# Kernel tuning notes

Measured on AMD Instinct MI355X. Metric: run time of the kernel, lower is better.

Reference implementation:

```python
import jax, jax.numpy as jnp
import numpy as np

D_MODEL = 1024
NUM_HEADS = 16
HEAD_DIM = D_MODEL // NUM_HEADS
D_FF = 4096
B, S = 4, 2048
EPS = 1e-5


def layernorm(x, gamma, beta):
    mu = jnp.mean(x, axis=-1, keepdims=True)
    var = jnp.mean(jnp.square(x - mu), axis=-1, keepdims=True)
    return (x - mu) * jax.lax.rsqrt(var + EPS) * gamma + beta


def setup_inputs() -> dict:
    key = jax.random.key(0)
    ks = jax.random.split(key, 16)
    s_in = 1.0 / np.sqrt(D_MODEL)
    s_ff = 1.0 / np.sqrt(D_FF)
    return {
        "x": jax.random.normal(ks[0], (B, S, D_MODEL), jnp.float32),
        "Wq": jax.random.normal(ks[1], (D_MODEL, D_MODEL), jnp.float32) * s_in,
        "bq": jnp.zeros((D_MODEL,), jnp.float32),
        "Wk": jax.random.normal(ks[2], (D_MODEL, D_MODEL), jnp.float32) * s_in,
        "bk": jnp.zeros((D_MODEL,), jnp.float32),
        "Wv": jax.random.normal(ks[3], (D_MODEL, D_MODEL), jnp.float32) * s_in,
        "bv": jnp.zeros((D_MODEL,), jnp.float32),
        "Wo": jax.random.normal(ks[4], (D_MODEL, D_MODEL), jnp.float32) * s_in,
        "bo": jnp.zeros((D_MODEL,), jnp.float32),
        "W1": jax.random.normal(ks[5], (D_MODEL, D_FF), jnp.float32) * s_in,
        "b1": jnp.zeros((D_FF,), jnp.float32),
        "W2": jax.random.normal(ks[6], (D_FF, D_MODEL), jnp.float32) * s_ff,
        "b2": jnp.zeros((D_MODEL,), jnp.float32),
        "g1": jnp.ones((D_MODEL,), jnp.float32),
        "be1": jnp.zeros((D_MODEL,), jnp.float32),
        "g2": jnp.ones((D_MODEL,), jnp.float32),
        "be2": jnp.zeros((D_MODEL,), jnp.float32),
    }


def reference(x, Wq, bq, Wk, bk, Wv, bv, Wo, bo, W1, b1, W2, b2, g1, be1, g2, be2):
    # multi-head self-attention (dropout is identity at eval)
    def split_heads(t):  # [B,S,D] -> [B,H,S,hd]
        return t.reshape(B, S, NUM_HEADS, HEAD_DIM).transpose(0, 2, 1, 3)

    q = split_heads(x @ Wq + bq)
    k = split_heads(x @ Wk + bk)
    v = split_heads(x @ Wv + bv)
    scores = jnp.einsum("bhqd,bhkd->bhqk", q, k) / np.sqrt(HEAD_DIM)
    attn = jax.nn.softmax(scores, axis=-1)
    out = jnp.einsum("bhqk,bhkd->bhqd", attn, v)
    out = out.transpose(0, 2, 1, 3).reshape(B, S, D_MODEL)
    attn_out = out @ Wo + bo

    h = layernorm(x + attn_out, g1, be1)
    ff = jax.nn.relu(h @ W1 + b1) @ W2 + b2
    return layernorm(h + ff, g2, be2)
```

## Files before the change

### kernel.cpp

```cpp
#include <hip/hip_runtime.h>
#include <hip/hip_bf16.h>


#define DM    1024
#define DFF   4096
#define NH    16
#define HD    64
#define BATCH 4
#define SEQ   2048
#define TOK   (BATCH * SEQ)

typedef __attribute__((ext_vector_type(8))) __bf16 bf16x8;
typedef __attribute__((ext_vector_type(4))) float f32x4;
typedef __attribute__((ext_vector_type(16))) float f32x16;
typedef __attribute__((ext_vector_type(4))) unsigned short u16x4;

typedef const __attribute__((address_space(1))) unsigned int* gas1_t;
typedef __attribute__((address_space(3))) unsigned int* las3_t;

__device__ __forceinline__ void gl_lds16(const void* g, void* l) {
  __builtin_amdgcn_global_load_lds((gas1_t)g, (las3_t)l, 16, 0, 0);
}

__device__ __forceinline__ unsigned short f2bu(float x) {
  return __builtin_bit_cast(unsigned short, __float2bfloat16(x));
}

__device__ __forceinline__ unsigned pk_bf16_trunc(float hi, float lo) {
  return __builtin_amdgcn_perm(__builtin_bit_cast(unsigned, hi),
                               __builtin_bit_cast(unsigned, lo), 0x07060302u);
}

__global__ __launch_bounds__(256) void cast_bf16(
    const float* __restrict__ in, unsigned short* __restrict__ out, int n4) {
  int i = blockIdx.x * 256 + threadIdx.x;
  if (i >= n4) return;
  float4 v = ((const float4*)in)[i];
  u16x4 o = {f2bu(v.x), f2bu(v.y), f2bu(v.z), f2bu(v.w)};
  ((u16x4*)out)[i] = o;
}

__global__ __launch_bounds__(256) void transpose_cast(
    const float* __restrict__ in, unsigned short* __restrict__ out, int K, int N) {
  __shared__ float tile[32][33];
  int n0 = blockIdx.x * 32, k0 = blockIdx.y * 32;
  int tx = threadIdx.x, ty = threadIdx.y;
#pragma unroll
  for (int i = 0; i < 4; ++i)
    tile[ty + 8 * i][tx] = in[(size_t)(k0 + ty + 8 * i) * N + n0 + tx];
  __syncthreads();
#pragma unroll
  for (int i = 0; i < 4; ++i)
    out[(size_t)(n0 + ty + 8 * i) * K + k0 + tx] = f2bu(tile[tx][ty + 8 * i]);
}

__global__ __launch_bounds__(256) void transpose_cast4(
    const float* __restrict__ A0, const float* __restrict__ A1,
    const float* __restrict__ A2, const float* __restrict__ A3,
    unsigned short* __restrict__ O0, unsigned short* __restrict__ O1,
    unsigned short* __restrict__ O2, unsigned short* __restrict__ O3) {
  __shared__ float tile[32][33];
  const float* in; unsigned short* out;
  switch (blockIdx.z) {
    case 0: in = A0; out = O0; break;
    case 1: in = A1; out = O1; break;
    case 2: in = A2; out = O2; break;
    default: in = A3; out = O3; break;
  }
  int n0 = blockIdx.x * 32, k0 = blockIdx.y * 32;
  int tx = threadIdx.x, ty = threadIdx.y;
#pragma unroll
  for (int i = 0; i < 4; ++i)
    tile[ty + 8 * i][tx] = in[(size_t)(k0 + ty + 8 * i) * DM + n0 + tx];
  __syncthreads();
#pragma unroll
  for (int i = 0; i < 4; ++i)
    out[(size_t)(n0 + ty + 8 * i) * DM + k0 + tx] = f2bu(tile[tx][ty + 8 * i]);
}

template <int QM, int QN>
__device__ __forceinline__ void phase_mma(
    const unsigned short* As, const unsigned short* Bs, int bufofs,
    int wr, int wc, int l31, int khalf, f32x16 acc[2][2][2]) {
  const char* Ah = (const char*)(As + bufofs + QM * 8192);
  const char* Bh = (const char*)(Bs + bufofs + QN * 8192);
  const int rA0 = wr * 64 + l31, rA1 = rA0 + 32, rB = wc * 32 + l31;
  bf16x8 a0[4], a1[4], bb[4];
#pragma unroll
  for (int ks = 0; ks < 4; ++ks) {
    const int c = ks * 2 + khalf;
    a0[ks] = *(const bf16x8*)(Ah + rA0 * 128 + ((c ^ (rA0 & 7)) << 4));
    a1[ks] = *(const bf16x8*)(Ah + rA1 * 128 + ((c ^ (rA1 & 7)) << 4));
    bb[ks] = *(const bf16x8*)(Bh + rB * 128 + ((c ^ (rB & 7)) << 4));
  }
  __builtin_amdgcn_s_setprio(1);
#pragma unroll
  for (int ks = 0; ks < 4; ++ks) {
    acc[QM][QN][0] = __builtin_amdgcn_mfma_f32_32x32x16_bf16(
        a0[ks], bb[ks], acc[QM][QN][0], 0, 0, 0);
    acc[QM][QN][1] = __builtin_amdgcn_mfma_f32_32x32x16_bf16(
        a1[ks], bb[ks], acc[QM][QN][1], 0, 0, 0);
  }
  __builtin_amdgcn_s_setprio(0);
}

__device__ __forceinline__ void mainloop256(
    const unsigned short* __restrict__ A, int lda,
    const unsigned short* __restrict__ Bt, int ldb, int Kl,
    int m0, int n0, unsigned short* As, unsigned short* Bs,
    f32x16 acc[2][2][2]) {
  const int tid = threadIdx.x, lane = tid & 63, w = tid >> 6;
  const int l31 = lane & 31, khalf = lane >> 5;
  const int wr = w >> 2, wc = w & 3;

  const unsigned short* pa[2][2];
  const unsigned short* pb[2][2];
#pragma unroll
  for (int h = 0; h < 2; ++h)
#pragma unroll
    for (int i = 0; i < 2; ++i) {
      const int g = (i * 8 + w) * 64 + lane;
      const int r = g >> 3;
      const int cs = ((g & 7) ^ (r & 7)) * 8;
      pa[h][i] = A + (size_t)(m0 + h * 128 + r) * lda + cs;
      pb[h][i] = Bt + (size_t)(n0 + h * 128 + r) * ldb + cs;
    }
  const int wofs = w * 512;

#define STA(BUF, H, I) gl_lds16(pa[H][I], As + (BUF) * 16384 + (H) * 8192 + (I) * 4096 + wofs)
#define STB(BUF, H, I) gl_lds16(pb[H][I], Bs + (BUF) * 16384 + (H) * 8192 + (I) * 4096 + wofs)
#define ADV_A(H) { pa[H][0] += 64; pa[H][1] += 64; }
#define ADV_B(H) { pb[H][0] += 64; pb[H][1] += 64; }

  STA(0, 0, 0); STA(0, 0, 1); ADV_A(0);
  STB(0, 0, 0); STB(0, 0, 1); ADV_B(0);
  STB(0, 1, 0); STB(0, 1, 1); ADV_B(1);
  STA(0, 1, 0); STA(0, 1, 1); ADV_A(1);

#define PH(BUF, QMv, QNv, WAITSTR, STG)                                  \
  asm volatile(WAITSTR ::: "memory");                                    \
  STG;                                                                   \
  phase_mma<QMv, QNv>(As, Bs, (BUF) * 16384, wr, wc, l31, khalf, acc)

#define TILE_STEADY(B)                                                        \
  PH(B, 0, 0, "s_waitcnt vmcnt(4)\n\ts_barrier",                              \
     { STA(B ^ 1, 0, 0); STA(B ^ 1, 0, 1); ADV_A(0); });                      \
  PH(B, 0, 1, "s_waitcnt vmcnt(4)\n\ts_barrier",                              \
     { STB(B ^ 1, 0, 0); STB(B ^ 1, 0, 1); ADV_B(0); });                      \
  PH(B, 1, 0, "s_waitcnt vmcnt(4)\n\ts_barrier",                              \
     { STB(B ^ 1, 1, 0); STB(B ^ 1, 1, 1); ADV_B(1); });                      \
  PH(B, 1, 1, "s_barrier",                                                    \
     { STA(B ^ 1, 1, 0); STA(B ^ 1, 1, 1); ADV_A(1); })

  const int NT = Kl >> 6;
  for (int t = 0; t + 2 < NT; t += 2) {
    TILE_STEADY(0);
    TILE_STEADY(1);
  }
  TILE_STEADY(0);
  PH(1, 0, 0, "s_waitcnt vmcnt(4)\n\ts_barrier", {});
  PH(1, 0, 1, "s_waitcnt vmcnt(2)\n\ts_barrier", {});
  PH(1, 1, 0, "s_waitcnt vmcnt(0)\n\ts_barrier", {});
  PH(1, 1, 1, "s_barrier", {});

#undef TILE_STEADY
#undef PH
#undef ADV_B
#undef ADV_A
#undef STB
#undef STA
}


__global__ __launch_bounds__(512, 2) void gemm256(
    const unsigned short* __restrict__ A, int lda,
    const unsigned short* __restrict__ Bt, int ldb, int Kl,
    const float* __restrict__ bias, void* __restrict__ C0,
    void* __restrict__ C1, int N, float alpha, int relu, int ofp32) {
  __shared__ unsigned short As[32768];
  __shared__ unsigned short Bs[32768];
  const int tid = threadIdx.x, lane = tid & 63, w = tid >> 6;
  const int l31 = lane & 31, khalf = lane >> 5;
  const int wr = w >> 2, wc = w & 3;
  const int m0 = blockIdx.y * 256, n0 = blockIdx.x * 256;
  const int koff = blockIdx.z * Kl;
  void* Cout = blockIdx.z ? C1 : C0;
  const float* be = blockIdx.z ? nullptr : bias;

  f32x16 acc[2][2][2];
#pragma unroll
  for (int qm = 0; qm < 2; ++qm)
#pragma unroll
    for (int qn = 0; qn < 2; ++qn)
#pragma unroll
      for (int mi = 0; mi < 2; ++mi)
#pragma unroll
        for (int r = 0; r < 16; ++r) acc[qm][qn][mi][r] = 0.f;

  mainloop256(A + koff, lda, Bt + koff, ldb, Kl, m0, n0, As, Bs, acc);

#pragma unroll
  for (int qn = 0; qn < 2; ++qn) {
    const int col = n0 + qn * 128 + wc * 32 + l31;
    const float bvv = be ? be[col] : 0.f;
#pragma unroll
    for (int qm = 0; qm < 2; ++qm)
#pragma unroll
      for (int mi = 0; mi < 2; ++mi) {
#pragma unroll
        for (int g = 0; g < 4; ++g) {
          const int rbase = m0 + qm * 128 + wr * 64 + mi * 32 + g * 8 + khalf * 4;
#pragma unroll
          for (int r = 0; r < 4; ++r) {
            float val = alpha * (acc[qm][qn][mi][g * 4 + r] + bvv);
            if (relu) val = fmaxf(val, 0.f);
            size_t idx = (size_t)(rbase + r) * N + col;
            if (ofp32) ((float*)Cout)[idx] = val;
            else ((unsigned short*)Cout)[idx] = f2bu(val);
          }
        }
      }
  }
}

#define QSCALE 0.18033688f

__global__ __launch_bounds__(512, 2) void gemm_qkv256(
    const unsigned short* __restrict__ A, const unsigned short* __restrict__ Bt,
    const float* __restrict__ bq, const float* __restrict__ bk,
    const float* __restrict__ bv,
    unsigned short* __restrict__ Qb, unsigned short* __restrict__ Kb,
    unsigned short* __restrict__ Vtg) {
  __shared__ unsigned short As[32768];
  __shared__ unsigned short Bs[32768];
  const int tid = threadIdx.x, lane = tid & 63, w = tid >> 6;
  const int l31 = lane & 31, khalf = lane >> 5;
  const int wr = w >> 2, wc = w & 3;
  const int m0 = blockIdx.y * 256, n0 = blockIdx.x * 256;

  f32x16 acc[2][2][2];
#pragma unroll
  for (int qm = 0; qm < 2; ++qm)
#pragma unroll
    for (int qn = 0; qn < 2; ++qn)
#pragma unroll
      for (int mi = 0; mi < 2; ++mi)
#pragma unroll
        for (int r = 0; r < 16; ++r) acc[qm][qn][mi][r] = 0.f;

  mainloop256(A, DM, Bt, DM, DM, m0, n0, As, Bs, acc);

  const int region = n0 >> 10;
  if (region < 2) {
    unsigned short* Out = region ? Kb : Qb;
    const float* bias = region ? bk : bq;
    const float alpha = region ? 1.0f : QSCALE;
#pragma unroll
    for (int qn = 0; qn < 2; ++qn) {
      const int col = (n0 & 1023) + qn * 128 + wc * 32 + l31;
      const float bvv = bias[col];
#pragma unroll
      for (int qm = 0; qm < 2; ++qm)
#pragma unroll
        for (int mi = 0; mi < 2; ++mi) {
#pragma unroll
          for (int g = 0; g < 4; ++g) {
            const int rbase = m0 + qm * 128 + wr * 64 + mi * 32 + g * 8 + khalf * 4;
#pragma unroll
            for (int r = 0; r < 4; ++r)
              Out[(size_t)(rbase + r) * DM + col] =
                  f2bu(alpha * (acc[qm][qn][mi][g * 4 + r] + bvv));
          }
        }
    }
  } else {
#pragma unroll
    for (int qn = 0; qn < 2; ++qn) {
      const int col = (n0 & 1023) + qn * 128 + wc * 32 + l31;
      const float bvv = bv[col];
      const int hh = col >> 6, dl = col & 63;
#pragma unroll
      for (int qm = 0; qm < 2; ++qm)
#pragma unroll
        for (int mi = 0; mi < 2; ++mi) {
#pragma unroll
          for (int g = 0; g < 4; ++g) {
            const int sbase = m0 + qm * 128 + wr * 64 + mi * 32 + g * 8 + khalf * 4;
            const int b_ = sbase >> 11, s0 = sbase & 2047;
            u16x4 pk;
#pragma unroll
            for (int r = 0; r < 4; ++r)
              pk[r] = f2bu(acc[qm][qn][mi][g * 4 + r] + bvv);
            *(u16x4*)(Vtg + ((size_t)((b_ * NH + hh) * HD + dl)) * SEQ + s0) = pk;
          }
        }
    }
  }
}

__global__ __launch_bounds__(256) void attn_kernel(
    const unsigned short* __restrict__ Q, const unsigned short* __restrict__ K,
    const unsigned short* __restrict__ Vtg, unsigned short* __restrict__ O) {
  __shared__ unsigned short Kt[2][64 * 64];
  __shared__ unsigned short Vt[2][64 * 64];
  __shared__ unsigned short Pt[4][32 * 64];
  __shared__ __align__(16) float redL[4][32];

  const int tid = threadIdx.x, lane = tid & 63, w = tid >> 6;
  const int l15 = lane & 15, quad = lane >> 4;
  const int q0 = blockIdx.x * 128;
  const int bh = blockIdx.y, b = bh >> 4, hh = bh & 15;
  const size_t tokbase = (size_t)b * SEQ;

  bf16x8 qf[2][2];
#pragma unroll
  for (int qg = 0; qg < 2; ++qg)
#pragma unroll
    for (int kk = 0; kk < 2; ++kk)
      qf[qg][kk] = *(const bf16x8*)(Q +
          (tokbase + q0 + w * 32 + qg * 16 + l15) * DM + hh * HD + kk * 32 + quad * 8);

  float l_run[2] = {0.f, 0.f};
  f32x4 Oacc[2][4];
#pragma unroll
  for (int qg = 0; qg < 2; ++qg)
#pragma unroll
    for (int nt = 0; nt < 4; ++nt) Oacc[qg][nt] = {0.f, 0.f, 0.f, 0.f};

  char* ptw = (char*)&Pt[w][0];

  int rowS[2], csrcS[2];
#pragma unroll
  for (int i = 0; i < 2; ++i) {
    int f = (i * 4 + w) * 64 + lane;
    rowS[i] = f >> 3;
    csrcS[i] = ((f & 7) ^ (rowS[i] & 7)) * 8;
  }
  const unsigned short* kg[2];
  const unsigned short* vg[2];
  char* ldsK[2][2]; char* ldsV[2][2];
#pragma unroll
  for (int i = 0; i < 2; ++i) {
    kg[i] = K + (tokbase + rowS[i]) * DM + hh * HD + csrcS[i];
    vg[i] = Vtg + ((size_t)bh * HD + rowS[i]) * SEQ + csrcS[i];
#pragma unroll
    for (int bb = 0; bb < 2; ++bb) {
      ldsK[bb][i] = (char*)Kt[bb] + (size_t)((i * 4 + w) * 1024);
      ldsV[bb][i] = (char*)Vt[bb] + (size_t)((i * 4 + w) * 1024);
    }
  }

#pragma unroll
  for (int i = 0; i < 2; ++i) {
    gl_lds16(kg[i], ldsK[0][i]);
    gl_lds16(vg[i], ldsV[0][i]);
    kg[i] += 64 * DM;
    vg[i] += 64;
  }

  for (int j = 0; j < SEQ / 64; ++j) {
    const int buf = j & 1;
    __syncthreads();
    if (j + 1 < SEQ / 64) {
#pragma unroll
      for (int i = 0; i < 2; ++i) {
        gl_lds16(kg[i], ldsK[buf ^ 1][i]);
        gl_lds16(vg[i], ldsV[buf ^ 1][i]);
        kg[i] += 64 * DM;
        vg[i] += 64;
      }
    }

    const char* ktb = (const char*)Kt[buf];
    const char* vtb = (const char*)Vt[buf];

    f32x4 S[2][4];
#pragma unroll
    for (int qg = 0; qg < 2; ++qg)
#pragma unroll
      for (int mt = 0; mt < 4; ++mt) S[qg][mt] = {0.f, 0.f, 0.f, 0.f};
#pragma unroll
    for (int kk = 0; kk < 2; ++kk) {
#pragma unroll
      for (int mt = 0; mt < 4; ++mt) {
        bf16x8 aK = *(const bf16x8*)(ktb + (mt * 16 + l15) * 128 +
                                     (((kk * 4 + quad) ^ (l15 & 7)) * 16));
        S[0][mt] = __builtin_amdgcn_mfma_f32_16x16x32_bf16(aK, qf[0][kk], S[0][mt], 0, 0, 0);
        S[1][mt] = __builtin_amdgcn_mfma_f32_16x16x32_bf16(aK, qf[1][kk], S[1][mt], 0, 0, 0);
      }
    }

#pragma unroll
    for (int qg = 0; qg < 2; ++qg) {
      float rs = 0.f;
#pragma unroll
      for (int mt = 0; mt < 4; ++mt) {
        float p0 = __builtin_amdgcn_exp2f(S[qg][mt][0]);
        float p1 = __builtin_amdgcn_exp2f(S[qg][mt][1]);
        float p2 = __builtin_amdgcn_exp2f(S[qg][mt][2]);
        float p3 = __builtin_amdgcn_exp2f(S[qg][mt][3]);
        rs += (p0 + p1) + (p2 + p3);
        uint2 pk = {pk_bf16_trunc(p1, p0), pk_bf16_trunc(p3, p2)};
        *(uint2*)(ptw + (qg * 16 + l15) * 128 +
                  (((mt * 2 + (quad >> 1)) ^ (l15 & 7)) * 16 + (quad & 1) * 8)) = pk;
      }
      l_run[qg] += rs;
    }

#pragma unroll
    for (int kk = 0; kk < 2; ++kk) {
      bf16x8 aP[2];
#pragma unroll
      for (int qg = 0; qg < 2; ++qg)
        aP[qg] = *(const bf16x8*)(ptw + (qg * 16 + l15) * 128 +
                                  (((kk * 4 + quad) ^ (l15 & 7)) * 16));
#pragma unroll
      for (int nt = 0; nt < 4; ++nt) {
        bf16x8 bV = *(const bf16x8*)(vtb + (nt * 16 + l15) * 128 +
                                     (((kk * 4 + quad) ^ (l15 & 7)) * 16));
        Oacc[0][nt] = __builtin_amdgcn_mfma_f32_16x16x32_bf16(aP[0], bV, Oacc[0][nt], 0, 0, 0);
        Oacc[1][nt] = __builtin_amdgcn_mfma_f32_16x16x32_bf16(aP[1], bV, Oacc[1][nt], 0, 0, 0);
      }
    }
  }

#pragma unroll
  for (int qg = 0; qg < 2; ++qg) {
    l_run[qg] += __shfl_xor(l_run[qg], 16);
    l_run[qg] += __shfl_xor(l_run[qg], 32);
    if (lane < 16) redL[w][qg * 16 + l15] = l_run[qg];
  }
#pragma unroll
  for (int qg = 0; qg < 2; ++qg) {
    f32x4 lv = *(const f32x4*)&redL[w][qg * 16 + quad * 4];
    f32x4 li;
#pragma unroll
    for (int r = 0; r < 4; ++r) li[r] = 1.0f / lv[r];
#pragma unroll
    for (int nt = 0; nt < 4; ++nt)
#pragma unroll
      for (int r = 0; r < 4; ++r) {
        size_t tok = tokbase + q0 + w * 32 + qg * 16 + quad * 4 + r;
        O[tok * DM + hh * HD + nt * 16 + l15] = f2bu(Oacc[qg][nt][r] * li[r]);
      }
  }
}

__global__ __launch_bounds__(256) void ln_res(
    const float* __restrict__ base, const float* __restrict__ d0,
    const float* __restrict__ d1,
    const float* __restrict__ gamma, const float* __restrict__ beta,
    float* __restrict__ outf, unsigned short* __restrict__ outb) {
  __shared__ float red[8];
  const int row = blockIdx.x, tid = threadIdx.x;
  const size_t rb = (size_t)row * DM;
  float4 xv = ((const float4*)(base + rb))[tid];
  float4 dv = ((const float4*)(d0 + rb))[tid];
  float s0 = xv.x + dv.x, s1 = xv.y + dv.y, s2 = xv.z + dv.z, s3 = xv.w + dv.w;
  if (d1) {
    float4 ev = ((const float4*)(d1 + rb))[tid];
    s0 += ev.x; s1 += ev.y; s2 += ev.z; s3 += ev.w;
  }
  float t = s0 + s1 + s2 + s3;
#pragma unroll
  for (int m = 1; m < 64; m <<= 1) t += __shfl_xor(t, m);
  if ((tid & 63) == 0) red[tid >> 6] = t;
  __syncthreads();
  float mu = (red[0] + red[1] + red[2] + red[3]) * (1.0f / DM);
  float dd0 = s0 - mu, dd1 = s1 - mu, dd2 = s2 - mu, dd3 = s3 - mu;
  float v = dd0 * dd0 + dd1 * dd1 + dd2 * dd2 + dd3 * dd3;
#pragma unroll
  for (int m = 1; m < 64; m <<= 1) v += __shfl_xor(v, m);
  if ((tid & 63) == 0) red[4 + (tid >> 6)] = v;
  __syncthreads();
  float var = (red[4] + red[5] + red[6] + red[7]) * (1.0f / DM);
  float rs = rsqrtf(var + 1e-5f);
  float4 gv = ((const float4*)gamma)[tid];
  float4 bv = ((const float4*)beta)[tid];
  float o0 = dd0 * rs * gv.x + bv.x;
  float o1 = dd1 * rs * gv.y + bv.y;
  float o2 = dd2 * rs * gv.z + bv.z;
  float o3 = dd3 * rs * gv.w + bv.w;
  float4 ov = {o0, o1, o2, o3};
  ((float4*)(outf + rb))[tid] = ov;
  if (outb) {
    u16x4 ob = {f2bu(o0), f2bu(o1), f2bu(o2), f2bu(o3)};
    ((u16x4*)(outb + rb))[tid] = ob;
  }
}

extern "C" void kernel_launch(void* const* d_in, const int* in_sizes, int n_in,
                              void* d_out, int out_size, void* d_ws, size_t ws_size,
                              hipStream_t stream) {
  const float* x   = (const float*)d_in[0];
  const float* Wq  = (const float*)d_in[1];  const float* bq  = (const float*)d_in[2];
  const float* Wk  = (const float*)d_in[3];  const float* bk  = (const float*)d_in[4];
  const float* Wv  = (const float*)d_in[5];  const float* bvv = (const float*)d_in[6];
  const float* Wo  = (const float*)d_in[7];  const float* bo  = (const float*)d_in[8];
  const float* W1  = (const float*)d_in[9];  const float* b1  = (const float*)d_in[10];
  const float* W2  = (const float*)d_in[11]; const float* b2  = (const float*)d_in[12];
  const float* g1  = (const float*)d_in[13]; const float* be1 = (const float*)d_in[14];
  const float* g2  = (const float*)d_in[15]; const float* be2 = (const float*)d_in[16];

  char* ws = (char*)d_ws;
  const size_t MB = 1ull << 20;
  unsigned short* xb    = (unsigned short*)(ws + 0 * MB);
  unsigned short* wqkvT = (unsigned short*)(ws + 16 * MB);
  unsigned short* woT   = (unsigned short*)(ws + 22 * MB);
  unsigned short* w1T   = (unsigned short*)(ws + 24 * MB);
  unsigned short* w2T   = (unsigned short*)(ws + 32 * MB);
  unsigned short* Qb    = (unsigned short*)(ws + 40 * MB);
  unsigned short* Kb    = (unsigned short*)(ws + 56 * MB);
  unsigned short* Vtg   = (unsigned short*)(ws + 72 * MB);
  unsigned short* aO    = (unsigned short*)(ws + 104 * MB);
  float*          prj   = (float*)(ws + 120 * MB);
  float*          h     = (float*)(ws + 152 * MB);
  unsigned short* hb    = (unsigned short*)(ws + 0 * MB);
  unsigned short* ffm   = (unsigned short*)(ws + 40 * MB);
  float*          ffo   = (float*)(ws + 104 * MB);
  float*          ffo2  = (float*)(ws + 0 * MB);
  (void)ws_size; (void)in_sizes; (void)n_in; (void)out_size;

  cast_bf16<<<TOK * DM / 4 / 256, 256, 0, stream>>>(x, xb, TOK * DM / 4);
  transpose_cast4<<<dim3(DM / 32, DM / 32, 4), dim3(32, 8), 0, stream>>>(
      Wq, Wk, Wv, Wo, wqkvT, wqkvT + 1024 * 1024, wqkvT + 2048 * 1024, woT);
  transpose_cast<<<dim3(DFF / 32, DM / 32), dim3(32, 8), 0, stream>>>(W1, w1T, DM, DFF);
  transpose_cast<<<dim3(DM / 32, DFF / 32), dim3(32, 8), 0, stream>>>(W2, w2T, DFF, DM);

  gemm_qkv256<<<dim3(3 * DM / 256, TOK / 256), 512, 0, stream>>>(
      xb, wqkvT, bq, bk, bvv, Qb, Kb, Vtg);

  attn_kernel<<<dim3(SEQ / 128, BATCH * NH), 256, 0, stream>>>(Qb, Kb, Vtg, aO);

  gemm256<<<dim3(DM / 256, TOK / 256, 1), 512, 0, stream>>>(
      aO, DM, woT, DM, DM, bo, prj, nullptr, DM, 1.0f, 0, 1);
  ln_res<<<TOK, 256, 0, stream>>>(x, prj, nullptr, g1, be1, h, hb);

  gemm256<<<dim3(DFF / 256, TOK / 256, 1), 512, 0, stream>>>(
      hb, DM, w1T, DM, DM, b1, ffm, nullptr, DFF, 1.0f, 1, 0);
  gemm256<<<dim3(DM / 256, TOK / 256, 2), 512, 0, stream>>>(
      ffm, DFF, w2T, DFF, DFF / 2, b2, ffo, ffo2, DM, 1.0f, 0, 1);

  ln_res<<<TOK, 256, 0, stream>>>(h, ffo, ffo2, g2, be2, (float*)d_out, nullptr);
}
```

Baseline: 639.7 us.

## Restructure GEMM mainloop with fragment reuse, XCD swizzle, and split-K Wo projection

Rewrites the 256x256 GEMM mainloop so that A and B fragments are loaded from LDS into registers and reused across quadrant MMAs, with fewer barriers per k-tile and retuned vmcnt waits. It adds an XCD-aware block-index swizzle to gemm256 and gemm_qkv256 to improve L2 locality per chiplet. The Wo projection is also split along K into two halves, giving more blocks to fill the GPU, and ln_res sums the two partial outputs. In exchange it uses more registers, the new waitcnt schedule has to stay correct, and the split-K path writes an extra fp32 partial buffer.

```diff
diff --git a/kernel.cpp b/kernel.cpp
--- a/kernel.cpp
+++ b/kernel.cpp
@@ -78,30 +78,10 @@
     out[(size_t)(n0 + ty + 8 * i) * DM + k0 + tx] = f2bu(tile[tx][ty + 8 * i]);
 }
 
-template <int QM, int QN>
-__device__ __forceinline__ void phase_mma(
-    const unsigned short* As, const unsigned short* Bs, int bufofs,
-    int wr, int wc, int l31, int khalf, f32x16 acc[2][2][2]) {
-  const char* Ah = (const char*)(As + bufofs + QM * 8192);
-  const char* Bh = (const char*)(Bs + bufofs + QN * 8192);
-  const int rA0 = wr * 64 + l31, rA1 = rA0 + 32, rB = wc * 32 + l31;
-  bf16x8 a0[4], a1[4], bb[4];
-#pragma unroll
-  for (int ks = 0; ks < 4; ++ks) {
-    const int c = ks * 2 + khalf;
-    a0[ks] = *(const bf16x8*)(Ah + rA0 * 128 + ((c ^ (rA0 & 7)) << 4));
-    a1[ks] = *(const bf16x8*)(Ah + rA1 * 128 + ((c ^ (rA1 & 7)) << 4));
-    bb[ks] = *(const bf16x8*)(Bh + rB * 128 + ((c ^ (rB & 7)) << 4));
-  }
-  __builtin_amdgcn_s_setprio(1);
-#pragma unroll
-  for (int ks = 0; ks < 4; ++ks) {
-    acc[QM][QN][0] = __builtin_amdgcn_mfma_f32_32x32x16_bf16(
-        a0[ks], bb[ks], acc[QM][QN][0], 0, 0, 0);
-    acc[QM][QN][1] = __builtin_amdgcn_mfma_f32_32x32x16_bf16(
-        a1[ks], bb[ks], acc[QM][QN][1], 0, 0, 0);
-  }
-  __builtin_amdgcn_s_setprio(0);
+__device__ __forceinline__ void mma8(const bf16x8 a0, const bf16x8 a1,
+                                     const bf16x8 b, f32x16* c0, f32x16* c1) {
+  *c0 = __builtin_amdgcn_mfma_f32_32x32x16_bf16(a0, b, *c0, 0, 0, 0);
+  *c1 = __builtin_amdgcn_mfma_f32_32x32x16_bf16(a1, b, *c1, 0, 0, 0);
 }
 
 __device__ __forceinline__ void mainloop256(
@@ -112,6 +92,7 @@
   const int tid = threadIdx.x, lane = tid & 63, w = tid >> 6;
   const int l31 = lane & 31, khalf = lane >> 5;
   const int wr = w >> 2, wc = w & 3;
+  const int rA0 = wr * 64 + l31, rA1 = rA0 + 32, rB = wc * 32 + l31;
 
   const unsigned short* pa[2][2];
   const unsigned short* pb[2][2];
@@ -125,52 +106,86 @@
       pa[h][i] = A + (size_t)(m0 + h * 128 + r) * lda + cs;
       pb[h][i] = Bt + (size_t)(n0 + h * 128 + r) * ldb + cs;
     }
-  const int wofs = w * 512;
-
-#define STA(BUF, H, I) gl_lds16(pa[H][I], As + (BUF) * 16384 + (H) * 8192 + (I) * 4096 + wofs)
-#define STB(BUF, H, I) gl_lds16(pb[H][I], Bs + (BUF) * 16384 + (H) * 8192 + (I) * 4096 + wofs)
+  const int wofsB = w * 1024;
+
+  bf16x8 aF[2][4], b0[4], b1[4];
+
+#define STA(BUF, H, I) \
+  gl_lds16(pa[H][I], (char*)As + (BUF) * 32768 + (H) * 16384 + (I) * 8192 + wofsB)
+#define STB(BUF, H, I) \
+  gl_lds16(pb[H][I], (char*)Bs + (BUF) * 32768 + (H) * 16384 + (I) * 8192 + wofsB)
 #define ADV_A(H) { pa[H][0] += 64; pa[H][1] += 64; }
 #define ADV_B(H) { pb[H][0] += 64; pb[H][1] += 64; }
 
-  STA(0, 0, 0); STA(0, 0, 1); ADV_A(0);
-  STB(0, 0, 0); STB(0, 0, 1); ADV_B(0);
-  STB(0, 1, 0); STB(0, 1, 1); ADV_B(1);
-  STA(0, 1, 0); STA(0, 1, 1); ADV_A(1);
-
-#define PH(BUF, QMv, QNv, WAITSTR, STG)                                  \
-  asm volatile(WAITSTR ::: "memory");                                    \
-  STG;                                                                   \
-  phase_mma<QMv, QNv>(As, Bs, (BUF) * 16384, wr, wc, l31, khalf, acc)
-
-#define TILE_STEADY(B)                                                        \
-  PH(B, 0, 0, "s_waitcnt vmcnt(4)\n\ts_barrier",                              \
-     { STA(B ^ 1, 0, 0); STA(B ^ 1, 0, 1); ADV_A(0); });                      \
-  PH(B, 0, 1, "s_waitcnt vmcnt(4)\n\ts_barrier",                              \
-     { STB(B ^ 1, 0, 0); STB(B ^ 1, 0, 1); ADV_B(0); });                      \
-  PH(B, 1, 0, "s_waitcnt vmcnt(4)\n\ts_barrier",                              \
-     { STB(B ^ 1, 1, 0); STB(B ^ 1, 1, 1); ADV_B(1); });                      \
-  PH(B, 1, 1, "s_barrier",                                                    \
-     { STA(B ^ 1, 1, 0); STA(B ^ 1, 1, 1); ADV_A(1); })
+#define RD_A(BUFB, H)                                                         \
+  { const char* Ah = (const char*)As + (BUFB) + (H) * 16384;                  \
+    _Pragma("unroll") for (int ks = 0; ks < 4; ++ks) {                        \
+      const int c = ks * 2 + khalf;                                           \
+      aF[0][ks] = *(const bf16x8*)(Ah + rA0 * 128 + ((c ^ (rA0 & 7)) << 4));  \
+      aF[1][ks] = *(const bf16x8*)(Ah + rA1 * 128 + ((c ^ (rA1 & 7)) << 4));  \
+    } }
+#define RD_B(DST, BUFB, H)                                                    \
+  { const char* Bh = (const char*)Bs + (BUFB) + (H) * 16384;                  \
+    _Pragma("unroll") for (int ks = 0; ks < 4; ++ks) {                        \
+      const int c = ks * 2 + khalf;                                           \
+      DST[ks] = *(const bf16x8*)(Bh + rB * 128 + ((c ^ (rB & 7)) << 4));      \
+    } }
+
+#define MMA4(QM, QN, BV)                                                      \
+  { __builtin_amdgcn_s_setprio(1);                                           \
+    _Pragma("unroll") for (int ks = 0; ks < 4; ++ks)                          \
+      mma8(aF[0][ks], aF[1][ks], BV[ks], &acc[QM][QN][0], &acc[QM][QN][1]);   \
+    __builtin_amdgcn_s_setprio(0); }
+
+#define TILE(BUF, STG, W0, W1, W3)                                            \
+  RD_A((BUF) * 32768, 0);                                                     \
+  RD_B(b0, (BUF) * 32768, 0);                                                 \
+  if (STG) { STA((BUF) ^ 1, 0, 0); STA((BUF) ^ 1, 0, 1); ADV_A(0);            \
+             STB((BUF) ^ 1, 0, 0); STB((BUF) ^ 1, 0, 1); ADV_B(0); }          \
+  asm volatile(W0 "\n\ts_barrier" ::: "memory");                              \
+  MMA4(0, 0, b0);                                                             \
+  RD_B(b1, (BUF) * 32768, 1);                                                 \
+  if (STG) { STB((BUF) ^ 1, 1, 0); STB((BUF) ^ 1, 1, 1); ADV_B(1); }          \
+  asm volatile(W1 "\n\ts_barrier" ::: "memory");                              \
+  MMA4(0, 1, b1);                                                             \
+  RD_A((BUF) * 32768, 1);                                                     \
+  if (STG) { STA((BUF) ^ 1, 1, 0); STA((BUF) ^ 1, 1, 1); ADV_A(1); }          \
+  MMA4(1, 1, b1);                                                             \
+  RD_B(b0, (BUF) * 32768, 0);                                                 \
+  asm volatile(W3 "\n\ts_barrier" ::: "memory");                              \
+  MMA4(1, 0, b0);
+
+  STA(0, 0, 0); STA(0, 0, 1); STB(0, 0, 0); STB(0, 0, 1);
+  STB(0, 1, 0); STB(0, 1, 1); STA(0, 1, 0); STA(0, 1, 1);
+  ADV_A(0); ADV_B(0); ADV_B(1); ADV_A(1);
+  asm volatile("s_waitcnt vmcnt(4)\n\ts_barrier" ::: "memory");
 
   const int NT = Kl >> 6;
   for (int t = 0; t + 2 < NT; t += 2) {
-    TILE_STEADY(0);
-    TILE_STEADY(1);
-  }
-  TILE_STEADY(0);
-  PH(1, 0, 0, "s_waitcnt vmcnt(4)\n\ts_barrier", {});
-  PH(1, 0, 1, "s_waitcnt vmcnt(2)\n\ts_barrier", {});
-  PH(1, 1, 0, "s_waitcnt vmcnt(0)\n\ts_barrier", {});
-  PH(1, 1, 1, "s_barrier", {});
-
-#undef TILE_STEADY
-#undef PH
+    TILE(0, 1, "s_waitcnt vmcnt(6)", "s_waitcnt vmcnt(6)", "s_waitcnt vmcnt(4)");
+    TILE(1, 1, "s_waitcnt vmcnt(6)", "s_waitcnt vmcnt(6)", "s_waitcnt vmcnt(4)");
+  }
+  TILE(0, 1, "s_waitcnt vmcnt(6)", "s_waitcnt vmcnt(6)", "s_waitcnt vmcnt(4)");
+  TILE(1, 0, "s_waitcnt vmcnt(2)", "s_waitcnt vmcnt(0)", "");
+
+#undef TILE
+#undef MMA4
+#undef RD_B
+#undef RD_A
 #undef ADV_B
 #undef ADV_A
 #undef STB
 #undef STA
 }
 
+
+__device__ __forceinline__ void xcd_swizzle(int& bx, int& by) {
+  const int gx = gridDim.x, nxy = gx * gridDim.y;
+  int lin = by * gx + bx;
+  lin = (lin & 7) * (nxy >> 3) + (lin >> 3);
+  bx = lin % gx;
+  by = lin / gx;
+}
 
 __global__ __launch_bounds__(512, 2) void gemm256(
     const unsigned short* __restrict__ A, int lda,
@@ -182,7 +197,9 @@
   const int tid = threadIdx.x, lane = tid & 63, w = tid >> 6;
   const int l31 = lane & 31, khalf = lane >> 5;
   const int wr = w >> 2, wc = w & 3;
-  const int m0 = blockIdx.y * 256, n0 = blockIdx.x * 256;
+  int bx = blockIdx.x, by = blockIdx.y;
+  xcd_swizzle(bx, by);
+  const int m0 = by * 256, n0 = bx * 256;
   const int koff = blockIdx.z * Kl;
   void* Cout = blockIdx.z ? C1 : C0;
   const float* be = blockIdx.z ? nullptr : bias;
@@ -236,7 +253,9 @@
   const int tid = threadIdx.x, lane = tid & 63, w = tid >> 6;
   const int l31 = lane & 31, khalf = lane >> 5;
   const int wr = w >> 2, wc = w & 3;
-  const int m0 = blockIdx.y * 256, n0 = blockIdx.x * 256;
+  int bx = blockIdx.x, by = blockIdx.y;
+  xcd_swizzle(bx, by);
+  const int m0 = by * 256, n0 = bx * 256;
 
   f32x16 acc[2][2][2];
 #pragma unroll
@@ -514,6 +533,7 @@
   unsigned short* Vtg   = (unsigned short*)(ws + 72 * MB);
   unsigned short* aO    = (unsigned short*)(ws + 104 * MB);
   float*          prj   = (float*)(ws + 120 * MB);
+  float*          prj2  = (float*)(ws + 40 * MB);
   float*          h     = (float*)(ws + 152 * MB);
   unsigned short* hb    = (unsigned short*)(ws + 0 * MB);
   unsigned short* ffm   = (unsigned short*)(ws + 40 * MB);
@@ -532,9 +552,9 @@
 
   attn_kernel<<<dim3(SEQ / 128, BATCH * NH), 256, 0, stream>>>(Qb, Kb, Vtg, aO);
 
-  gemm256<<<dim3(DM / 256, TOK / 256, 1), 512, 0, stream>>>(
-      aO, DM, woT, DM, DM, bo, prj, nullptr, DM, 1.0f, 0, 1);
-  ln_res<<<TOK, 256, 0, stream>>>(x, prj, nullptr, g1, be1, h, hb);
+  gemm256<<<dim3(DM / 256, TOK / 256, 2), 512, 0, stream>>>(
+      aO, DM, woT, DM, DM / 2, bo, prj, prj2, DM, 1.0f, 0, 1);
+  ln_res<<<TOK, 256, 0, stream>>>(x, prj, prj2, g1, be1, h, hb);
 
   gemm256<<<dim3(DFF / 256, TOK / 256, 1), 512, 0, stream>>>(
       hb, DM, w1T, DM, DM, b1, ffm, nullptr, DFF, 1.0f, 1, 0);
```

Result: faster. 593.9 us (-7.2%).
